# Performance work log

Measured on AMD Instinct MI355X. Metric: run time of the kernel, lower is better.

The kernel has to match this reference:

```python
import jax, jax.numpy as jnp
import numpy as np

N_COLORS = 3  # color1..color3 occupy z[:, 3:6]


def setup_inputs() -> dict:
    key = jax.random.key(0)
    k1, k2 = jax.random.split(key)
    B, D = 4194304, 8
    z = jax.random.normal(k1, (B, D), dtype=jnp.float32)
    a = jax.random.uniform(k2, (B, N_COLORS), dtype=jnp.float32)
    return {"z": z, "a": a}


def reference(z, a):
    # Vectorized equivalent of the per-row loop: argmax over the color slice,
    # one-hot it, mask with a, and reduce over the color axis.
    colors = z[:, 3:6]                                   # [B, 3]
    z_color = jax.nn.one_hot(jnp.argmax(colors, axis=1), N_COLORS, dtype=z.dtype)
    return (a * z_color).sum(axis=1)                     # [B]
```

## Files before the change

kernel.cpp:

```cpp
#include <hip/hip_runtime.h>
#include <hip/hip_bf16.h>


__global__ __launch_bounds__(256) void color_val_kernel(
    const float* __restrict__ z,
    const float* __restrict__ a,
    float* __restrict__ out,
    int nquads)
{
    int t = blockIdx.x * blockDim.x + threadIdx.x;
    if (t >= nquads) return;

    const float4* z4 = reinterpret_cast<const float4*>(z) + (size_t)t * 8;
    const float4* a4 = reinterpret_cast<const float4*>(a) + (size_t)t * 3;

    float4 zl[8];
#pragma unroll
    for (int k = 0; k < 8; ++k) zl[k] = z4[k];

    float4 av0 = a4[0];
    float4 av1 = a4[1];
    float4 av2 = a4[2];
    float aa[12] = {av0.x, av0.y, av0.z, av0.w,
                    av1.x, av1.y, av1.z, av1.w,
                    av2.x, av2.y, av2.z, av2.w};

    float4 o;
    float* op = &o.x;
#pragma unroll
    for (int r = 0; r < 4; ++r) {
        float c0 = zl[2 * r].w;
        float c1 = zl[2 * r + 1].x;
        float c2 = zl[2 * r + 1].y;
        float m   = c0;
        float val = aa[r * 3 + 0];
        if (c1 > m) { m = c1; val = aa[r * 3 + 1]; }
        if (c2 > m) {          val = aa[r * 3 + 2]; }
        op[r] = val;
    }

    reinterpret_cast<float4*>(out)[t] = o;
}

extern "C" void kernel_launch(void* const* d_in, const int* in_sizes, int n_in,
                              void* d_out, int out_size, void* d_ws, size_t ws_size,
                              hipStream_t stream) {
    const float* z = (const float*)d_in[0];
    const float* a = (const float*)d_in[1];
    float* out = (float*)d_out;

    int B = out_size;
    int nquads = B / 4;
    int block = 256;
    int grid = (nquads + block - 1) / block;
    color_val_kernel<<<grid, block, 0, stream>>>(z, a, out, nquads);
}
```

Before: 42.61 us.

## Stage z and a tiles through LDS for coalesced global loads

Each block now cooperatively loads 512 rows of z and a into shared memory with fully coalesced float4/float2 loads, then each thread picks the argmax color and writes one output per row. This aims to replace the per-thread strided 128-byte loads with coalesced wavefront accesses. It adds LDS traffic, a barrier, and padded scalar LDS stores, plus a separate tail kernel for leftover rows.

```diff
diff --git a/kernel.cpp b/kernel.cpp
--- a/kernel.cpp
+++ b/kernel.cpp
@@ -2,44 +2,71 @@
 #include <hip/hip_bf16.h>
 
 
-__global__ __launch_bounds__(256) void color_val_kernel(
+#define ROWS_PER_BLOCK 512
+#define NTHREADS 256
+
+__global__ __launch_bounds__(NTHREADS) void color_val_lds(
+    const float* __restrict__ z,
+    const float* __restrict__ a,
+    float* __restrict__ out)
+{
+    __shared__ __align__(16) float zs[ROWS_PER_BLOCK * 9];
+    __shared__ __align__(16) float as_[ROWS_PER_BLOCK * 3];
+
+    const int t = threadIdx.x;
+    const size_t rowBase = (size_t)blockIdx.x * ROWS_PER_BLOCK;
+
+    const float4* zg = reinterpret_cast<const float4*>(z) + rowBase * 2;
+#pragma unroll
+    for (int q = 0; q < 4; ++q) {
+        int f = q * NTHREADS + t;
+        float4 v = zg[f];
+        int r = f >> 1;
+        int h = (f & 1) * 4;
+        float* p = &zs[r * 9 + h];
+        p[0] = v.x; p[1] = v.y; p[2] = v.z; p[3] = v.w;
+    }
+
+    const float2* ag = reinterpret_cast<const float2*>(a) + (rowBase * 3) / 2;
+    float2* as2 = reinterpret_cast<float2*>(as_);
+#pragma unroll
+    for (int q = 0; q < 3; ++q) {
+        int p2 = q * NTHREADS + t;
+        as2[p2] = ag[p2];
+    }
+
+    __syncthreads();
+
+#pragma unroll
+    for (int k = 0; k < 2; ++k) {
+        int r = k * NTHREADS + t;
+        const float* zr = &zs[r * 9];
+        float c0 = zr[3];
+        float c1 = zr[4];
+        float c2 = zr[5];
+        const float* ar = &as_[r * 3];
+        float val = ar[0];
+        float m = c0;
+        if (c1 > m) { m = c1; val = ar[1]; }
+        if (c2 > m) {          val = ar[2]; }
+        out[rowBase + r] = val;
+    }
+}
+
+__global__ void color_val_tail(
     const float* __restrict__ z,
     const float* __restrict__ a,
     float* __restrict__ out,
-    int nquads)
+    size_t start, size_t B)
 {
-    int t = blockIdx.x * blockDim.x + threadIdx.x;
-    if (t >= nquads) return;
-
-    const float4* z4 = reinterpret_cast<const float4*>(z) + (size_t)t * 8;
-    const float4* a4 = reinterpret_cast<const float4*>(a) + (size_t)t * 3;
-
-    float4 zl[8];
-#pragma unroll
-    for (int k = 0; k < 8; ++k) zl[k] = z4[k];
-
-    float4 av0 = a4[0];
-    float4 av1 = a4[1];
-    float4 av2 = a4[2];
-    float aa[12] = {av0.x, av0.y, av0.z, av0.w,
-                    av1.x, av1.y, av1.z, av1.w,
-                    av2.x, av2.y, av2.z, av2.w};
-
-    float4 o;
-    float* op = &o.x;
-#pragma unroll
-    for (int r = 0; r < 4; ++r) {
-        float c0 = zl[2 * r].w;
-        float c1 = zl[2 * r + 1].x;
-        float c2 = zl[2 * r + 1].y;
-        float m   = c0;
-        float val = aa[r * 3 + 0];
-        if (c1 > m) { m = c1; val = aa[r * 3 + 1]; }
-        if (c2 > m) {          val = aa[r * 3 + 2]; }
-        op[r] = val;
-    }
-
-    reinterpret_cast<float4*>(out)[t] = o;
+    size_t i = start + blockIdx.x * blockDim.x + threadIdx.x;
+    if (i >= B) return;
+    float c0 = z[i * 8 + 3], c1 = z[i * 8 + 4], c2 = z[i * 8 + 5];
+    float val = a[i * 3 + 0];
+    float m = c0;
+    if (c1 > m) { m = c1; val = a[i * 3 + 1]; }
+    if (c2 > m) {          val = a[i * 3 + 2]; }
+    out[i] = val;
 }
 
 extern "C" void kernel_launch(void* const* d_in, const int* in_sizes, int n_in,
@@ -49,9 +76,15 @@
     const float* a = (const float*)d_in[1];
     float* out = (float*)d_out;
 
-    int B = out_size;
-    int nquads = B / 4;
-    int block = 256;
-    int grid = (nquads + block - 1) / block;
-    color_val_kernel<<<grid, block, 0, stream>>>(z, a, out, nquads);
+    size_t B = (size_t)out_size;
+    size_t nfull = B / ROWS_PER_BLOCK;
+    size_t rem = B % ROWS_PER_BLOCK;
+
+    if (nfull > 0)
+        color_val_lds<<<(int)nfull, NTHREADS, 0, stream>>>(z, a, out);
+    if (rem > 0) {
+        size_t start = nfull * ROWS_PER_BLOCK;
+        int blocks = (int)((rem + 255) / 256);
+        color_val_tail<<<blocks, 256, 0, stream>>>(z, a, out, start, B);
+    }
 }
```

Measured after the change: 34.29 us. 1.24x faster.
